# Kernel tuning notes

Measured on AMD Instinct MI355X. Metric: run time of the kernel, lower is better.

The kernel has to match this reference:

```python
import jax, jax.numpy as jnp
import numpy as np
from itertools import permutations

B, T, S = 32, 65536, 4
EPS = 1e-7
PIT_W, VAD_W = 1.0, 0.5
PERMS = np.array(list(permutations(range(S))), dtype=np.int32)  # [24, 4]


def setup_inputs() -> dict:
    key = jax.random.key(0)
    k1, k2, k3, k4, k5 = jax.random.split(key, 5)
    pred_speakers = jax.random.uniform(k1, (B, T, S), dtype=jnp.float32)
    pred_vad = jax.random.uniform(k2, (B, T), dtype=jnp.float32)
    labels = jax.random.randint(k3, (B, T, S), 0, 2).astype(jnp.float32)
    vad = jax.random.randint(k4, (B, T), 0, 2).astype(jnp.float32)
    lengths = jnp.maximum(jax.random.randint(k5, (B,), 0, T), T // 2).astype(jnp.int64)
    return {"pred_speakers": pred_speakers, "pred_vad": pred_vad,
            "labels": labels, "vad": vad, "lengths": lengths}


def reference(pred_speakers, pred_vad, labels, vad, lengths):
    mask = (jnp.arange(T)[None, :] < lengths[:, None]).astype(jnp.float32)  # [B,T]
    msum = mask.sum(axis=1)  # [B]

    # --- PIT speaker loss (num_speakers=4 -> exact permutation search) ---
    p = jnp.clip(pred_speakers, EPS, 1.0 - EPS)
    lp = jnp.log(p)          # log p
    lq = jnp.log1p(-p)       # log(1-p)
    # pairwise masked BCE cost: L[b,i,j] = sum_t mask * bce(pred_i, target_j) / sum_t mask
    #   bce = -(t*lp + (1-t)*lq) = -t*(lp-lq) - lq
    mt = labels * mask[:, :, None]                              # [B,T,S]
    term1 = -jnp.einsum('bti,btj->bij', lp - lq, mt)            # [B,S,S]
    term2 = -(lq * mask[:, :, None]).sum(axis=1)                # [B,S]
    L = (term1 + term2[:, :, None]) / msum[:, None, None]       # [B,S,S]
    perms = jnp.asarray(PERMS)                                  # [24,S]
    # perm_loss[b,p] = mean_i L[b, i, perms[p,i]]
    perm_losses = L[:, jnp.arange(S)[None, :], perms].mean(axis=-1)  # [B,24]
    speaker_loss = perm_losses.min(axis=1).mean()

    # --- VAD BCE loss ---
    pv = jnp.clip(pred_vad, EPS, 1.0 - EPS)
    bce_v = -(vad * jnp.log(pv) + (1.0 - vad) * jnp.log1p(-pv))
    vad_loss = (bce_v * mask).sum() / mask.sum()

    return PIT_W * speaker_loss + VAD_W * vad_loss
```

## Files before the change

### kernel.cpp

```cpp
#include <hip/hip_runtime.h>

#define B 32
#define T 65536
#define S 4
#define EPSF 1e-7f
#define TPB 256
#define CHUNK 2048
#define NCHUNK (T / CHUNK)
#define NBLK (B * NCHUNK)
#define NACC 21

__device__ __forceinline__ float wave_reduce_sum(float v) {
    #pragma unroll
    for (int off = 32; off > 0; off >>= 1) v += __shfl_down(v, off, 64);
    return v;
}

__global__ void init_kernel(float* acc, unsigned int* done) {
    for (int k = threadIdx.x; k < B * NACC; k += 256) acc[k] = 0.0f;
    if (threadIdx.x == 0) *done = 0u;
}

__global__ __launch_bounds__(TPB) void fused_kernel(
    const float4* __restrict__ ps,
    const float*  __restrict__ pv,
    const float4* __restrict__ lb,
    const float*  __restrict__ vd,
    const int*    __restrict__ len,
    float* __restrict__ acc,
    unsigned int* __restrict__ done,
    float* __restrict__ out)
{
    const int b  = blockIdx.x / NCHUNK;
    const int c  = blockIdx.x % NCHUNK;
    const int t0 = c * CHUNK;
    const int L  = len[b];

    if (t0 < L) {
        const int tend = min(t0 + CHUNK, L);

        float a1[16], a2[4], av = 0.0f;
        #pragma unroll
        for (int k = 0; k < 16; ++k) a1[k] = 0.0f;
        #pragma unroll
        for (int k = 0; k < 4; ++k)  a2[k] = 0.0f;

        const int base = b * T;
        for (int t = t0 + (int)threadIdx.x; t < tend; t += TPB) {
            const float4 p4 = ps[base + t];
            const float4 l4 = lb[base + t];
            const float p[4] = {p4.x, p4.y, p4.z, p4.w};
            const float l[4] = {l4.x, l4.y, l4.z, l4.w};
            float d[4];
            #pragma unroll
            for (int i = 0; i < 4; ++i) {
                const float pc = fminf(fmaxf(p[i], EPSF), 1.0f - EPSF);
                const float lp = __logf(pc);
                const float lq = __logf(1.0f - pc);
                a2[i] += lq;
                d[i] = lp - lq;
            }
            #pragma unroll
            for (int i = 0; i < 4; ++i)
                #pragma unroll
                for (int j = 0; j < 4; ++j)
                    a1[i * 4 + j] = fmaf(d[i], l[j], a1[i * 4 + j]);

            const float pvc = fminf(fmaxf(pv[base + t], EPSF), 1.0f - EPSF);
            const float v   = vd[base + t];
            av += __logf((v > 0.5f) ? pvc : (1.0f - pvc));
        }

        __shared__ float smem[TPB / 64][NACC];
        const int lane = threadIdx.x & 63;
        const int wv   = threadIdx.x >> 6;

        float vals[NACC];
        #pragma unroll
        for (int k = 0; k < 16; ++k) vals[k] = a1[k];
        #pragma unroll
        for (int k = 0; k < 4; ++k)  vals[16 + k] = a2[k];
        vals[20] = av;

        #pragma unroll
        for (int k = 0; k < NACC; ++k) {
            const float r = wave_reduce_sum(vals[k]);
            if (lane == 0) smem[wv][k] = r;
        }
        __syncthreads();
        if (threadIdx.x < NACC) {
            float s = 0.0f;
            #pragma unroll
            for (int w = 0; w < TPB / 64; ++w) s += smem[w][threadIdx.x];
            atomicAdd(&acc[b * NACC + threadIdx.x], s);
            __threadfence();
        }
    }

    __shared__ unsigned int s_old;
    __syncthreads();
    if (threadIdx.x == 0) s_old = atomicAdd(done, 1u);
    __syncthreads();

    if (s_old == (unsigned int)(NBLK - 1)) {
        const int tid = threadIdx.x;
        if (tid < 64) {
            float best = 0.0f, vadn = 0.0f, lensum = 0.0f;
            if (tid < B) {
                const int bb = tid;
                const float msum = (float)len[bb];
                float t2[4];
                #pragma unroll
                for (int i = 0; i < 4; ++i)
                    t2[i] = atomicAdd(&acc[bb * NACC + 16 + i], 0.0f);
                float Lm[16];
                #pragma unroll
                for (int i = 0; i < 4; ++i)
                    #pragma unroll
                    for (int j = 0; j < 4; ++j)
                        Lm[i * 4 + j] =
                            (-atomicAdd(&acc[bb * NACC + i * 4 + j], 0.0f) - t2[i]) / msum;

                best = 1e30f;
                #pragma unroll
                for (int p0 = 0; p0 < 4; ++p0)
                    #pragma unroll
                    for (int p1 = 0; p1 < 4; ++p1) {
                        if (p1 == p0) continue;
                        #pragma unroll
                        for (int p2 = 0; p2 < 4; ++p2) {
                            if (p2 == p0 || p2 == p1) continue;
                            const int p3 = 6 - p0 - p1 - p2;
                            best = fminf(best,
                                Lm[p0] + Lm[4 + p1] + Lm[8 + p2] + Lm[12 + p3]);
                        }
                    }
                best *= 0.25f;
                vadn   = -atomicAdd(&acc[bb * NACC + 20], 0.0f);
                lensum = msum;
            }
            best   = wave_reduce_sum(best);
            vadn   = wave_reduce_sum(vadn);
            lensum = wave_reduce_sum(lensum);
            if (tid == 0)
                out[0] = best * (1.0f / B) + 0.5f * (vadn / lensum);
        }
    }
}

extern "C" void kernel_launch(void* const* d_in, const int* in_sizes, int n_in,
                              void* d_out, int out_size, void* d_ws, size_t ws_size,
                              hipStream_t stream) {
    const float4* ps  = (const float4*)d_in[0];
    const float*  pv  = (const float*)d_in[1];
    const float4* lb  = (const float4*)d_in[2];
    const float*  vd  = (const float*)d_in[3];
    const int*    len = (const int*)d_in[4];
    float*        acc = (float*)d_ws;
    unsigned int* done = (unsigned int*)((char*)d_ws + B * NACC * sizeof(float));
    float*        out = (float*)d_out;

    init_kernel<<<1, 256, 0, stream>>>(acc, done);
    fused_kernel<<<NBLK, TPB, 0, stream>>>(ps, pv, lb, vd, len, acc, done, out);
}
```

Baseline: 127.6 us.

## Replace atomic accumulation and last-block finish with per-chunk partials and final kernel

Removes the init kernel, the global float atomics and the done-counter ticket. Each block now writes its 21 partial sums to a dedicated workspace slot, and a separate single-block kernel reduces them and runs the permutation search. The chunk size drops so each thread handles exactly two timesteps with loads issued up front, giving four times as many blocks for more memory parallelism. The cost is more blocks doing a per-block reduction and a larger partial buffer that the final kernel must read.

```diff
diff --git a/kernel.cpp b/kernel.cpp
--- a/kernel.cpp
+++ b/kernel.cpp
@@ -2,12 +2,11 @@
 
 #define B 32
 #define T 65536
-#define S 4
 #define EPSF 1e-7f
 #define TPB 256
-#define CHUNK 2048
-#define NCHUNK (T / CHUNK)
-#define NBLK (B * NCHUNK)
+#define CHUNK 512
+#define NCHUNKB (T / CHUNK)
+#define NBLK (B * NCHUNKB)
 #define NACC 21
 
 __device__ __forceinline__ float wave_reduce_sum(float v) {
@@ -16,135 +15,150 @@
     return v;
 }
 
-__global__ void init_kernel(float* acc, unsigned int* done) {
-    for (int k = threadIdx.x; k < B * NACC; k += 256) acc[k] = 0.0f;
-    if (threadIdx.x == 0) *done = 0u;
+__device__ __forceinline__ void accum_t(float4 p4, float4 l4, float pvv, float vdd,
+                                        float (&a1)[16], float (&a2)[4], float& av) {
+    const float p[4] = {p4.x, p4.y, p4.z, p4.w};
+    const float l[4] = {l4.x, l4.y, l4.z, l4.w};
+    float d[4];
+    #pragma unroll
+    for (int i = 0; i < 4; ++i) {
+        const float pc = fminf(fmaxf(p[i], EPSF), 1.0f - EPSF);
+        const float lp = __logf(pc);
+        const float lq = __logf(1.0f - pc);
+        a2[i] += lq;
+        d[i] = lp - lq;
+    }
+    #pragma unroll
+    for (int i = 0; i < 4; ++i)
+        #pragma unroll
+        for (int j = 0; j < 4; ++j)
+            a1[i * 4 + j] = fmaf(d[i], l[j], a1[i * 4 + j]);
+    const float pvc = fminf(fmaxf(pvv, EPSF), 1.0f - EPSF);
+    av += __logf((vdd > 0.5f) ? pvc : (1.0f - pvc));
 }
 
-__global__ __launch_bounds__(TPB) void fused_kernel(
+__global__ __launch_bounds__(TPB) void main_kernel(
     const float4* __restrict__ ps,
     const float*  __restrict__ pv,
     const float4* __restrict__ lb,
     const float*  __restrict__ vd,
     const int*    __restrict__ len,
-    float* __restrict__ acc,
-    unsigned int* __restrict__ done,
+    float* __restrict__ part)
+{
+    const int b  = blockIdx.x >> 7;
+    const int c  = blockIdx.x & (NCHUNKB - 1);
+    const int t0 = c * CHUNK;
+    const int L  = len[b];
+    const int tid = threadIdx.x;
+
+    float a1[16], a2[4], av = 0.0f;
+    #pragma unroll
+    for (int k = 0; k < 16; ++k) a1[k] = 0.0f;
+    #pragma unroll
+    for (int k = 0; k < 4; ++k)  a2[k] = 0.0f;
+
+    if (t0 < L) {
+        const int base = b * T;
+        if (t0 + CHUNK <= L) {
+            const int ta = base + t0 + tid;
+            const int tb2 = ta + TPB;
+            const float4 P0 = ps[ta],  P1 = ps[tb2];
+            const float4 L0 = lb[ta],  L1 = lb[tb2];
+            const float  v0 = pv[ta],  v1 = pv[tb2];
+            const float  w0 = vd[ta],  w1 = vd[tb2];
+            accum_t(P0, L0, v0, w0, a1, a2, av);
+            accum_t(P1, L1, v1, w1, a1, a2, av);
+        } else {
+            #pragma unroll
+            for (int u = 0; u < 2; ++u) {
+                const int t = t0 + tid + u * TPB;
+                if (t < L) {
+                    const int g = b * T + t;
+                    accum_t(ps[g], lb[g], pv[g], vd[g], a1, a2, av);
+                }
+            }
+        }
+    }
+
+    __shared__ float smem[TPB / 64][NACC];
+    const int lane = tid & 63;
+    const int wv   = tid >> 6;
+
+    float vals[NACC];
+    #pragma unroll
+    for (int k = 0; k < 16; ++k) vals[k] = a1[k];
+    #pragma unroll
+    for (int k = 0; k < 4; ++k)  vals[16 + k] = a2[k];
+    vals[20] = av;
+
+    #pragma unroll
+    for (int k = 0; k < NACC; ++k) {
+        const float r = wave_reduce_sum(vals[k]);
+        if (lane == 0) smem[wv][k] = r;
+    }
+    __syncthreads();
+    if (tid < NACC) {
+        float s = 0.0f;
+        #pragma unroll
+        for (int w = 0; w < TPB / 64; ++w) s += smem[w][tid];
+        part[(b * NACC + tid) * NCHUNKB + c] = s;
+    }
+}
+
+__global__ __launch_bounds__(704) void final_kernel(
+    const float* __restrict__ part,
+    const int*   __restrict__ len,
     float* __restrict__ out)
 {
-    const int b  = blockIdx.x / NCHUNK;
-    const int c  = blockIdx.x % NCHUNK;
-    const int t0 = c * CHUNK;
-    const int L  = len[b];
+    __shared__ float sums[B][NACC];
+    const int tid = threadIdx.x;
 
-    if (t0 < L) {
-        const int tend = min(t0 + CHUNK, L);
+    if (tid < B * NACC) {
+        const float4* p4 = (const float4*)(part + (size_t)tid * NCHUNKB);
+        float4 a = {0.f, 0.f, 0.f, 0.f};
+        #pragma unroll
+        for (int i = 0; i < NCHUNKB / 4; ++i) {
+            const float4 v = p4[i];
+            a.x += v.x; a.y += v.y; a.z += v.z; a.w += v.w;
+        }
+        sums[tid / NACC][tid % NACC] = (a.x + a.y) + (a.z + a.w);
+    }
+    __syncthreads();
 
-        float a1[16], a2[4], av = 0.0f;
-        #pragma unroll
-        for (int k = 0; k < 16; ++k) a1[k] = 0.0f;
-        #pragma unroll
-        for (int k = 0; k < 4; ++k)  a2[k] = 0.0f;
-
-        const int base = b * T;
-        for (int t = t0 + (int)threadIdx.x; t < tend; t += TPB) {
-            const float4 p4 = ps[base + t];
-            const float4 l4 = lb[base + t];
-            const float p[4] = {p4.x, p4.y, p4.z, p4.w};
-            const float l[4] = {l4.x, l4.y, l4.z, l4.w};
-            float d[4];
-            #pragma unroll
-            for (int i = 0; i < 4; ++i) {
-                const float pc = fminf(fmaxf(p[i], EPSF), 1.0f - EPSF);
-                const float lp = __logf(pc);
-                const float lq = __logf(1.0f - pc);
-                a2[i] += lq;
-                d[i] = lp - lq;
-            }
+    if (tid < 64) {
+        float best = 0.0f, vadn = 0.0f, lensum = 0.0f;
+        if (tid < B) {
+            const int bb = tid;
+            const float msum = (float)len[bb];
+            float Lm[16];
             #pragma unroll
             for (int i = 0; i < 4; ++i)
                 #pragma unroll
                 for (int j = 0; j < 4; ++j)
-                    a1[i * 4 + j] = fmaf(d[i], l[j], a1[i * 4 + j]);
+                    Lm[i * 4 + j] = (-sums[bb][i * 4 + j] - sums[bb][16 + i]) / msum;
 
-            const float pvc = fminf(fmaxf(pv[base + t], EPSF), 1.0f - EPSF);
-            const float v   = vd[base + t];
-            av += __logf((v > 0.5f) ? pvc : (1.0f - pvc));
+            best = 1e30f;
+            #pragma unroll
+            for (int p0 = 0; p0 < 4; ++p0)
+                #pragma unroll
+                for (int p1 = 0; p1 < 4; ++p1) {
+                    if (p1 == p0) continue;
+                    #pragma unroll
+                    for (int p2 = 0; p2 < 4; ++p2) {
+                        if (p2 == p0 || p2 == p1) continue;
+                        const int p3 = 6 - p0 - p1 - p2;
+                        best = fminf(best, Lm[p0] + Lm[4 + p1] + Lm[8 + p2] + Lm[12 + p3]);
+                    }
+                }
+            best *= 0.25f;
+            vadn   = -sums[bb][20];
+            lensum = msum;
         }
-
-        __shared__ float smem[TPB / 64][NACC];
-        const int lane = threadIdx.x & 63;
-        const int wv   = threadIdx.x >> 6;
-
-        float vals[NACC];
-        #pragma unroll
-        for (int k = 0; k < 16; ++k) vals[k] = a1[k];
-        #pragma unroll
-        for (int k = 0; k < 4; ++k)  vals[16 + k] = a2[k];
-        vals[20] = av;
-
-        #pragma unroll
-        for (int k = 0; k < NACC; ++k) {
-            const float r = wave_reduce_sum(vals[k]);
-            if (lane == 0) smem[wv][k] = r;
-        }
-        __syncthreads();
-        if (threadIdx.x < NACC) {
-            float s = 0.0f;
-            #pragma unroll
-            for (int w = 0; w < TPB / 64; ++w) s += smem[w][threadIdx.x];
-            atomicAdd(&acc[b * NACC + threadIdx.x], s);
-            __threadfence();
-        }
-    }
-
-    __shared__ unsigned int s_old;
-    __syncthreads();
-    if (threadIdx.x == 0) s_old = atomicAdd(done, 1u);
-    __syncthreads();
-
-    if (s_old == (unsigned int)(NBLK - 1)) {
-        const int tid = threadIdx.x;
-        if (tid < 64) {
-            float best = 0.0f, vadn = 0.0f, lensum = 0.0f;
-            if (tid < B) {
-                const int bb = tid;
-                const float msum = (float)len[bb];
-                float t2[4];
-                #pragma unroll
-                for (int i = 0; i < 4; ++i)
-                    t2[i] = atomicAdd(&acc[bb * NACC + 16 + i], 0.0f);
-                float Lm[16];
-                #pragma unroll
-                for (int i = 0; i < 4; ++i)
-                    #pragma unroll
-                    for (int j = 0; j < 4; ++j)
-                        Lm[i * 4 + j] =
-                            (-atomicAdd(&acc[bb * NACC + i * 4 + j], 0.0f) - t2[i]) / msum;
-
-                best = 1e30f;
-                #pragma unroll
-                for (int p0 = 0; p0 < 4; ++p0)
-                    #pragma unroll
-                    for (int p1 = 0; p1 < 4; ++p1) {
-                        if (p1 == p0) continue;
-                        #pragma unroll
-                        for (int p2 = 0; p2 < 4; ++p2) {
-                            if (p2 == p0 || p2 == p1) continue;
-                            const int p3 = 6 - p0 - p1 - p2;
-                            best = fminf(best,
-                                Lm[p0] + Lm[4 + p1] + Lm[8 + p2] + Lm[12 + p3]);
-                        }
-                    }
-                best *= 0.25f;
-                vadn   = -atomicAdd(&acc[bb * NACC + 20], 0.0f);
-                lensum = msum;
-            }
-            best   = wave_reduce_sum(best);
-            vadn   = wave_reduce_sum(vadn);
-            lensum = wave_reduce_sum(lensum);
-            if (tid == 0)
-                out[0] = best * (1.0f / B) + 0.5f * (vadn / lensum);
-        }
+        best   = wave_reduce_sum(best);
+        vadn   = wave_reduce_sum(vadn);
+        lensum = wave_reduce_sum(lensum);
+        if (tid == 0)
+            out[0] = best * (1.0f / B) + 0.5f * (vadn / lensum);
     }
 }
 
@@ -156,10 +170,9 @@
     const float4* lb  = (const float4*)d_in[2];
     const float*  vd  = (const float*)d_in[3];
     const int*    len = (const int*)d_in[4];
-    float*        acc = (float*)d_ws;
-    unsigned int* done = (unsigned int*)((char*)d_ws + B * NACC * sizeof(float));
-    float*        out = (float*)d_out;
+    float*        part = (float*)d_ws;
+    float*        out  = (float*)d_out;
 
-    init_kernel<<<1, 256, 0, stream>>>(acc, done);
-    fused_kernel<<<NBLK, TPB, 0, stream>>>(ps, pv, lb, vd, len, acc, done, out);
+    main_kernel<<<NBLK, TPB, 0, stream>>>(ps, pv, lb, vd, len, part);
+    final_kernel<<<1, 704, 0, stream>>>(part, len, out);
 }
```

New measurement: 135.3 us. +6.0%, slower.
